# Performance work log

Hardware: AMD Instinct MI355X
Metric: run time of the kernel (lower is better)

The kernel has to match this reference:

```python
import jax, jax.numpy as jnp
import numpy as np

D = 64        # embedding_dim
H = 16        # embedding_dim // 4
DAY = 86400.0
N_USERS = 200000
T_TOTAL = 8400000


def _mlp(x, w1, b1, w2, b2):
    return jax.nn.relu(x @ w1 + b1) @ w2 + b2


def setup_inputs() -> dict:
    key = jax.random.key(0)
    ks = jax.random.split(key, 20)
    N, T = N_USERS, T_TOTAL
    # every user gets >= 3 check-ins, rest assigned randomly
    base = np.tile(np.arange(N, dtype=np.int32), 3)
    rnd = np.asarray(jax.random.randint(ks[0], (T - 3 * N,), 0, N, dtype=jnp.int32))
    segment_ids = jnp.asarray(np.sort(np.concatenate([base, rnd])).astype(np.int32))
    # quantized coordinates so per-user unique-row counting is meaningful
    locations = jnp.round(jax.random.normal(ks[1], (T, 2), jnp.float32) * 50.0) / 50.0
    timestamps = jax.random.uniform(ks[2], (T,), jnp.float32, 0.0, 1.0e7)
    categories = jax.random.randint(ks[3], (T,), 0, 10, dtype=jnp.int32)

    def lin(k, din, dout):
        kw, kb = jax.random.split(k)
        w = jax.random.normal(kw, (din, dout), jnp.float32) / np.float32(np.sqrt(din))
        b = jax.random.normal(kb, (dout,), jnp.float32) * 0.01
        return w, b

    p = {}
    ki = 4
    for nm, din in [("loc", 2), ("tmp", 3), ("act", 10), ("mob", 4)]:
        p[f"w_{nm}1"], p[f"b_{nm}1"] = lin(ks[ki], din, H); ki += 1
        p[f"w_{nm}2"], p[f"b_{nm}2"] = lin(ks[ki], H, H); ki += 1
    p["w_cmb1"], p["b_cmb1"] = lin(ks[ki], D, D); ki += 1
    p["w_cmb2"], p["b_cmb2"] = lin(ks[ki], D, D)
    return dict(locations=locations, timestamps=timestamps,
                categories=categories, segment_ids=segment_ids, num_users=N, **p)


def reference(locations, timestamps,
              w_loc1, b_loc1, w_loc2, b_loc2,
              w_tmp1, b_tmp1, w_tmp2, b_tmp2,
              w_act1, b_act1, w_act2, b_act2,
              w_mob1, b_mob1, w_mob2, b_mob2,
              w_cmb1, b_cmb1, w_cmb2, b_cmb2,
              categories, segment_ids, num_users):
    seg, N = segment_ids, num_users
    ss = lambda v: jax.ops.segment_sum(v, seg, num_segments=N, indices_are_sorted=True)
    L = ss(jnp.ones_like(timestamps))                        # [N] check-ins per user

    # home location = mean over user's locations
    home = ss(locations) / L[:, None]                        # [N, 2]

    # temporal patterns: mean hour / day / month
    hours = jnp.mod(timestamps, DAY) / 3600.0
    days = jnp.mod(timestamps / DAY, 7.0)
    months = jnp.mod(timestamps / (30.0 * DAY), 12.0)
    tmp = ss(jnp.stack([hours, days, months], -1)) / L[:, None]   # [N, 3]

    # activity distribution over 10 POI categories
    hist = jnp.zeros((N, 10), locations.dtype).at[seg, categories].add(1.0)
    hs = hist.sum(-1, keepdims=True)
    act = jnp.where(hs > 0, hist / jnp.maximum(hs, 1.0), hist)    # [N, 10]

    # mobility stats: radius = std (ddof=1) of distance to centroid
    d = jnp.linalg.norm(locations - home[seg], axis=1)
    dmean = ss(d) / L
    radius = jnp.sqrt(ss((d - dmean[seg]) ** 2) / (L - 1.0))

    # diversity: unique locations per user via segment-local lexsort
    x, y = locations[:, 0], locations[:, 1]
    order = jnp.lexsort((y, x, seg))
    sx, sy, sseg = x[order], y[order], seg[order]
    new = jnp.concatenate([jnp.ones((1,), bool),
                           (sseg[1:] != sseg[:-1]) | (sx[1:] != sx[:-1]) | (sy[1:] != sy[:-1])])
    uniq = jax.ops.segment_sum(new.astype(locations.dtype), sseg,
                               num_segments=N, indices_are_sorted=True)
    diversity = uniq / L

    # frequency: check-ins per day of time span
    tmax = jax.ops.segment_max(timestamps, seg, num_segments=N, indices_are_sorted=True)
    tmin = jax.ops.segment_min(timestamps, seg, num_segments=N, indices_are_sorted=True)
    span = (tmax - tmin) / DAY
    freq = L / jnp.maximum(span, 1.0)

    # regularity: 1 / (std(consecutive time diffs, ddof=1) + 1e-6)
    diffs = timestamps[1:] - timestamps[:-1]
    same = seg[1:] == seg[:-1]
    seg1 = seg[1:]
    ss1 = lambda v: jax.ops.segment_sum(v, seg1, num_segments=N, indices_are_sorted=True)
    m = L - 1.0                                              # diffs per user
    dmu = ss1(jnp.where(same, diffs, 0.0)) / m
    dvar = ss1(jnp.where(same, (diffs - dmu[seg1]) ** 2, 0.0)) / (m - 1.0)
    reg = 1.0 / (jnp.sqrt(dvar) + 1e-6)

    mob = jnp.stack([radius, diversity, freq, reg], -1)      # [N, 4]

    feats = jnp.concatenate([
        _mlp(home, w_loc1, b_loc1, w_loc2, b_loc2),
        _mlp(tmp, w_tmp1, b_tmp1, w_tmp2, b_tmp2),
        _mlp(act, w_act1, b_act1, w_act2, b_act2),
        _mlp(mob, w_mob1, b_mob1, w_mob2, b_mob2),
    ], -1)                                                   # [N, 64]
    return _mlp(feats, w_cmb1, b_cmb1, w_cmb2, b_cmb2)       # [N, 64]
```

## Files before the change

kernel.cpp:

```cpp
#include <hip/hip_runtime.h>

typedef short bf16x8 __attribute__((ext_vector_type(8)));
typedef float f32x4 __attribute__((ext_vector_type(4)));

struct Params {
  const float* loc; const float* ts; const int* cat; const int* seg;
  const int* off;
  const float *wl1,*bl1,*wl2,*bl2;
  const float *wt1,*bt1,*wt2,*bt2;
  const float *wa1,*ba1,*wa2,*ba2;
  const float *wm1,*bm1,*wm2,*bm2;
  const float *wc1,*bc1,*wc2,*bc2;
  float* out;
  unsigned* wfrag;
  int N, T, use_off;
};

__global__ void offsets_kernel(const int* __restrict__ seg, int* __restrict__ off, int T, int N) {
  int i = blockIdx.x * blockDim.x + threadIdx.x;
  if (i == 0) off[N] = T;
  if (i < T) {
    int s = seg[i];
    if (i == 0 || seg[i-1] != s) off[s] = i;
  }
}

__device__ __forceinline__ int rdlane_i(int v, int l) {
  return __builtin_amdgcn_readlane(v, l);
}
__device__ __forceinline__ float rdlane_f(float v, int l) {
  return __int_as_float(__builtin_amdgcn_readlane(__float_as_int(v), l));
}

__device__ __forceinline__ unsigned bf16r(float f) {
  unsigned x = __float_as_uint(f);
  return (x + 0x7fffu + ((x >> 16) & 1u)) >> 16;
}
__device__ __forceinline__ unsigned pack_hl(float f) {
  unsigned hi = bf16r(f);
  float r = f - __uint_as_float(hi << 16);
  return (hi << 16) | bf16r(r);
}

__device__ __forceinline__ float exact_fmod(float a, float m, float rcp_m) {
  float q = floorf(a * rcp_m);
  float r = fmaf(q, -m, a);
  if (r < 0.0f) r += m;
  else if (r >= m) r -= m;
  return r;
}

__device__ __forceinline__ f32x4 mfma16(bf16x8 a, bf16x8 b, f32x4 c) {
  return __builtin_amdgcn_mfma_f32_16x16x32_bf16(a, b, c, 0, 0, 0);
}

__device__ __forceinline__ void lda(const unsigned* rp, bf16x8& hi, bf16x8& lo) {
  uint4 w0 = *(const uint4*)rp;
  uint4 w1 = *(const uint4*)(rp + 4);
  union { unsigned u[4]; bf16x8 v; } H, L;
  H.u[0] = __builtin_amdgcn_perm(w0.y, w0.x, 0x07060302u);
  H.u[1] = __builtin_amdgcn_perm(w0.w, w0.z, 0x07060302u);
  H.u[2] = __builtin_amdgcn_perm(w1.y, w1.x, 0x07060302u);
  H.u[3] = __builtin_amdgcn_perm(w1.w, w1.z, 0x07060302u);
  L.u[0] = __builtin_amdgcn_perm(w0.y, w0.x, 0x05040100u);
  L.u[1] = __builtin_amdgcn_perm(w0.w, w0.z, 0x05040100u);
  L.u[2] = __builtin_amdgcn_perm(w1.y, w1.x, 0x05040100u);
  L.u[3] = __builtin_amdgcn_perm(w1.w, w1.z, 0x05040100u);
  hi = H.v; lo = L.v;
}

__device__ __forceinline__ float bdval_(const float* wl2, const float* wt2,
                                        const float* wa2, const float* wm2,
                                        int k, int col) {
  if ((k >> 4) != (col >> 4)) return 0.f;
  int b = col >> 4;
  const float* W2 = (b & 2) ? ((b & 1) ? wm2 : wa2) : ((b & 1) ? wt2 : wl2);
  return W2[(k & 15) * 16 + (col & 15)];
}

__device__ __forceinline__ unsigned frag_word(const Params& p, int m) {
  int fi = m >> 8;
  int ln = (m >> 2) & 63;
  int j2 = m & 3;
  int layer, nt, ks;
  if (fi < 4)       { layer = 0; nt = fi;             ks = nt >> 1; }
  else if (fi < 12) { layer = 1; nt = (fi - 4) >> 1;  ks = (fi - 4) & 1; }
  else              { layer = 2; nt = (fi - 12) >> 1; ks = (fi - 12) & 1; }
  int col = nt * 16 + (ln & 15);
  int k0  = ks * 32 + ((ln >> 4) << 3) + (j2 << 1);
  float v0, v1;
  if (layer == 0) {
    v0 = bdval_(p.wl2, p.wt2, p.wa2, p.wm2, k0, col);
    v1 = bdval_(p.wl2, p.wt2, p.wa2, p.wm2, k0 + 1, col);
  } else {
    const float* W = (layer == 1) ? p.wc1 : p.wc2;
    v0 = W[k0 * 64 + col]; v1 = W[(k0 + 1) * 64 + col];
  }
  return (bf16r(v1) << 16) | bf16r(v0);
}

__global__ void pack_kernel(Params p) {
  int m = blockIdx.x * 256 + threadIdx.x;
  if (m < 5120) p.wfrag[m] = frag_word(p, m);
}

__device__ __forceinline__ bf16x8 g_ldb(const Params& p, int fi, int lane) {
  union { uint4 q; unsigned u[4]; bf16x8 v; } U;
  if (p.wfrag) {
    U.q = *(const uint4*)(p.wfrag + ((fi * 64 + lane) << 2));
  } else {
    int m = fi * 256 + lane * 4;
    U.u[0] = frag_word(p, m + 0);
    U.u[1] = frag_word(p, m + 1);
    U.u[2] = frag_word(p, m + 2);
    U.u[3] = frag_word(p, m + 3);
  }
  return U.v;
}

__device__ __forceinline__ int lower_bound(const int* seg, int T, int v) {
  int lo = 0, hi = T;
  while (lo < hi) { int m = (lo + hi) >> 1; if (seg[m] < v) lo = m + 1; else hi = m; }
  return lo;
}

__device__ __forceinline__ float pscan_f(float v) {
  v += __int_as_float(__builtin_amdgcn_update_dpp(0, __float_as_int(v), 0x111, 0xf, 0xf, true));
  v += __int_as_float(__builtin_amdgcn_update_dpp(0, __float_as_int(v), 0x112, 0xf, 0xf, true));
  v += __int_as_float(__builtin_amdgcn_update_dpp(0, __float_as_int(v), 0x114, 0xf, 0xf, true));
  v += __int_as_float(__builtin_amdgcn_update_dpp(0, __float_as_int(v), 0x118, 0xf, 0xf, true));
  v += __int_as_float(__builtin_amdgcn_update_dpp(0, __float_as_int(v), 0x142, 0xa, 0xf, true));
  v += __int_as_float(__builtin_amdgcn_update_dpp(0, __float_as_int(v), 0x143, 0xc, 0xf, true));
  return v;
}
__device__ __forceinline__ unsigned pscan_u(unsigned v) {
  int x = (int)v;
  x += __builtin_amdgcn_update_dpp(0, x, 0x111, 0xf, 0xf, true);
  x += __builtin_amdgcn_update_dpp(0, x, 0x112, 0xf, 0xf, true);
  x += __builtin_amdgcn_update_dpp(0, x, 0x114, 0xf, 0xf, true);
  x += __builtin_amdgcn_update_dpp(0, x, 0x118, 0xf, 0xf, true);
  x += __builtin_amdgcn_update_dpp(0, x, 0x142, 0xa, 0xf, true);
  x += __builtin_amdgcn_update_dpp(0, x, 0x143, 0xc, 0xf, true);
  return (unsigned)x;
}
__device__ __forceinline__ unsigned wshr1_u(unsigned v) {
  return (unsigned)__builtin_amdgcn_update_dpp(0, (int)v, 0x138, 0xf, 0xf, true);
}
__device__ __forceinline__ float wshr1_f(float v) {
  return __int_as_float(__builtin_amdgcn_update_dpp(0, __float_as_int(v), 0x138, 0xf, 0xf, true));
}

__global__ __launch_bounds__(256, 4) void mobility_kernel(Params p) {
  __shared__ __align__(16) unsigned s_pool[4352];
  __shared__ float s_w1[304];
  __shared__ float s_b1[64], s_b2[64], s_bc1[64], s_bc2[64];

  int tid = threadIdx.x;
  int lane = tid & 63, w = tid >> 6;

  if (tid < 32)  s_w1[tid]       = p.wl1[tid];
  if (tid < 48)  s_w1[32 + tid]  = p.wt1[tid];
  if (tid < 160) s_w1[80 + tid]  = p.wa1[tid];
  if (tid < 64)  s_w1[240 + tid] = p.wm1[tid];
  if (tid < 16) {
    s_b1[tid]    = p.bl1[tid]; s_b1[16+tid] = p.bt1[tid];
    s_b1[32+tid] = p.ba1[tid]; s_b1[48+tid] = p.bm1[tid];
    s_b2[tid]    = p.bl2[tid]; s_b2[16+tid] = p.bt2[tid];
    s_b2[32+tid] = p.ba2[tid]; s_b2[48+tid] = p.bm2[tid];
  }
  if (tid < 64) { s_bc1[tid] = p.bc1[tid]; s_bc2[tid] = p.bc2[tid]; }
  __syncthreads();

  int uw0 = blockIdx.x * 64 + w * 16;
  if (uw0 >= p.N) return;
  int myu = uw0 + lane;
  int myuc = min(myu, p.N - 1);
  int s0, e0;
  if (p.use_off) {
    s0 = p.off[myuc]; e0 = p.off[myuc + 1];
  } else {
    s0 = lower_bound(p.seg, p.T, myuc);
    e0 = lower_bound(p.seg, p.T, myuc + 1);
  }
  int W0 = rdlane_i(s0, 0);
  int W1 = rdlane_i(e0, 15);
  float Lf = (float)(e0 - s0);

  const float2* lp2 = (const float2*)p.loc;
  const float NINF = __int_as_float(0xff800000u);
  const float PINF = __int_as_float(0x7f800000u);

  int aKx = 0, aKy = 0, aXX = 0;
  float aH = 0.f, aDY = 0.f, aT = 0.f, aDF2 = 0.f;
  unsigned aH0 = 0u, aH1 = 0u, aH2 = 0u;

  for (int base = W0; base < W1; base += 64) {
    int e = base + lane;
    bool on = e < W1;
    int ec = on ? e : (W1 - 1);
    int sv = p.seg[ec];
    int sn = (ec + 1 < p.T) ? p.seg[ec + 1] : -2;
    float t  = p.ts[ec];
    float tnx = (ec + 1 < p.T) ? p.ts[ec + 1] : 0.f;
    int c = p.cat[ec];
    float2 xy = lp2[ec];

    unsigned vXY = 0u, vXX = 0u, vH0 = 0u, vH1 = 0u, vH2 = 0u;
    float vH = 0.f, vDY = 0.f, vT = 0.f, vDF2 = 0.f;
    if (on) {
      int kx = (int)lrintf(xy.x * 50.0f);
      int ky = (int)lrintf(xy.y * 50.0f);
      vXY = ((unsigned)(kx + 512) << 16) | (unsigned)(ky + 512);
      vXX = (unsigned)(kx * kx + ky * ky);
      float hr = exact_fmod(t, 86400.0f, 1.0f / 86400.0f);
      vH = hr * (1.0f / 3600.0f);
      float ud = (float)((double)t * (1.0 / 86400.0));
      vDY = exact_fmod(ud, 7.0f, 1.0f / 7.0f);
      vT = t;
      unsigned bit = 1u << ((c & 3) * 8);
      int wsel = c >> 2;
      vH0 = (wsel == 0) ? bit : 0u;
      vH1 = (wsel == 1) ? bit : 0u;
      vH2 = (wsel == 2) ? bit : 0u;
      if (sn == sv) { float dt = tnx - t; vDF2 = dt * dt; }
    }

    unsigned pXY = pscan_u(vXY), pXX = pscan_u(vXX);
    unsigned pH0 = pscan_u(vH0), pH1 = pscan_u(vH1), pH2 = pscan_u(vH2);
    float pH = pscan_f(vH), pDY = pscan_f(vDY), pT = pscan_f(vT), pDF2 = pscan_f(vDF2);

    int lo = min(max(s0 - base, 0), 64);
    int hi = min(max(e0 - base, 0), 64);
    int idx = max(hi - 1, 0);
    unsigned PXY = (unsigned)__shfl((int)pXY, idx);
    unsigned PXX = (unsigned)__shfl((int)pXX, idx);
    unsigned PH0 = (unsigned)__shfl((int)pH0, idx);
    unsigned PH1 = (unsigned)__shfl((int)pH1, idx);
    unsigned PH2 = (unsigned)__shfl((int)pH2, idx);
    float PH = __shfl(pH, idx), PDY = __shfl(pDY, idx);
    float PT = __shfl(pT, idx), PDF2 = __shfl(pDF2, idx);
    unsigned LXY = wshr1_u(PXY), LXX = wshr1_u(PXX);
    unsigned LH0 = wshr1_u(PH0), LH1 = wshr1_u(PH1), LH2 = wshr1_u(PH2);
    float LH = wshr1_f(PH), LDY = wshr1_f(PDY);
    float LT = wshr1_f(PT), LDF2 = wshr1_f(PDF2);

    if (hi > lo) {
      int cnt = hi - lo;
      bool ul_ = lo > 0;
      unsigned dXY = PXY - (ul_ ? LXY : 0u);
      aKx += (int)(dXY >> 16) - (cnt << 9);
      aKy += (int)(dXY & 0xffffu) - (cnt << 9);
      aXX += (int)(PXX - (ul_ ? LXX : 0u));
      aH0 += PH0 - (ul_ ? LH0 : 0u);
      aH1 += PH1 - (ul_ ? LH1 : 0u);
      aH2 += PH2 - (ul_ ? LH2 : 0u);
      aH   += PH   - (ul_ ? LH   : 0.f);
      aDY  += PDY  - (ul_ ? LDY  : 0.f);
      aT   += PT   - (ul_ ? LT   : 0.f);
      aDF2 += PDF2 - (ul_ ? LDF2 : 0.f);
    }
  }

  float hx, hy;
  {
    float sx = (float)aKx / 50.0f, sy = (float)aKy / 50.0f;
    hx = sx / Lf; hy = sy / Lf;
  }

  unsigned* fw = s_pool + w * 1088;
  unsigned* hashp = fw;
  float uqf = 0.f, tmxA = NINF, tmnA = PINF, aD = 0.f;
  for (int uu = 0; uu < 16; ++uu) {
    if (uw0 + uu >= p.N) break;
    int suu = rdlane_i(s0, uu), euu = rdlane_i(e0, uu);
    float hxu = rdlane_f(hx, uu), hyu = rdlane_f(hy, uu);
    int Lu = euu - suu;
    int uq = 0;
    float cmx = NINF, cmn = PINF, dsum = 0.f;
    if (Lu <= 96) {
      hashp[lane] = 0u; hashp[64 + lane] = 0u;
      asm volatile("s_waitcnt lgkmcnt(0)" ::: "memory");
      for (int b2 = suu; b2 < euu; b2 += 64) {
        int i = b2 + lane;
        bool fresh = false;
        if (i < euu) {
          float tv = p.ts[i];
          cmx = fmaxf(cmx, tv); cmn = fminf(cmn, tv);
          float2 xy = lp2[i];
          float dx = xy.x - hxu, dyv = xy.y - hyu;
          dsum += sqrtf(fmaf(dx, dx, dyv * dyv));
          int kx = (int)lrintf(xy.x * 50.0f) + 2048;
          int ky = (int)lrintf(xy.y * 50.0f) + 2048;
          unsigned key = (((unsigned)kx << 12) | (unsigned)ky) + 1u;
          unsigned h = (key * 2654435761u) >> 25;
          while (true) {
            unsigned old = atomicCAS(&hashp[h], 0u, key);
            if (old == 0u) { fresh = true; break; }
            if (old == key) break;
            h = (h + 1) & 127u;
          }
        }
        uq += (int)__popcll(__ballot(fresh));
      }
    } else {
      for (int b2 = suu; b2 < euu; b2 += 64) {
        int i = b2 + lane;
        bool fresh = false;
        if (i < euu) {
          float tv = p.ts[i];
          cmx = fmaxf(cmx, tv); cmn = fminf(cmn, tv);
          float x = p.loc[2*(size_t)i], y = p.loc[2*(size_t)i+1];
          float dx = x - hxu, dyv = y - hyu;
          dsum += sqrtf(fmaf(dx, dx, dyv * dyv));
          fresh = true;
          for (int jj = suu; jj < i; ++jj) {
            if (p.loc[2*(size_t)jj] == x && p.loc[2*(size_t)jj+1] == y) { fresh = false; break; }
          }
        }
        uq += (int)__popcll(__ballot(fresh));
      }
    }
    #pragma unroll
    for (int o = 32; o > 0; o >>= 1) {
      cmx = fmaxf(cmx, __shfl_xor(cmx, o));
      cmn = fminf(cmn, __shfl_xor(cmn, o));
      dsum += __shfl_xor(dsum, o);
    }
    if (lane == uu) { uqf = (float)uq; tmxA = cmx; tmnA = cmn; aD = dsum; }
  }
  asm volatile("s_waitcnt lgkmcnt(0)" ::: "memory");

  int lr = lane & 15, g2 = lane >> 4;
  int us0 = __shfl(s0, lr), ue0 = __shfl(e0, lr);
  float LfU = (float)(ue0 - us0);
  int KX = __shfl(aKx, lr), KY = __shfl(aKy, lr), XX = __shfl(aXX, lr);
  float H_ = __shfl(aH, lr), DY_ = __shfl(aDY, lr);
  float T_ = __shfl(aT, lr), DF2_ = __shfl(aDF2, lr);
  unsigned H0_ = (unsigned)__shfl((int)aH0, lr);
  unsigned H1_ = (unsigned)__shfl((int)aH1, lr);
  unsigned H2_ = (unsigned)__shfl((int)aH2, lr);
  float TMX_ = __shfl(tmxA, lr), TMN_ = __shfl(tmnA, lr);
  float D_ = __shfl(aD, lr), UQ_ = __shfl(uqf, lr);

  unsigned hp16[16];
  if (g2 == 0) {
    float sxU = (float)KX / 50.0f, syU = (float)KY / 50.0f;
    float hxU = sxU / LfU, hyU = syU / LfU;
    #pragma unroll
    for (int j = 0; j < 16; ++j)
      hp16[j] = pack_hl(fmaxf(s_b1[j] + hxU * s_w1[j] + hyU * s_w1[16 + j], 0.f));
  } else if (g2 == 1) {
    float th = H_ / LfU, tdy = DY_ / LfU;
    float tmo = (T_ * (1.0f / 2592000.0f)) / LfU;
    #pragma unroll
    for (int j = 0; j < 16; ++j)
      hp16[j] = pack_hl(fmaxf(s_b1[16 + j] + th * s_w1[32 + j] + tdy * s_w1[48 + j]
                              + tmo * s_w1[64 + j], 0.f));
  } else if (g2 == 2) {
    float act[10];
    act[0] = (float)(H0_ & 255u) / LfU;
    act[1] = (float)((H0_ >> 8) & 255u) / LfU;
    act[2] = (float)((H0_ >> 16) & 255u) / LfU;
    act[3] = (float)((H0_ >> 24) & 255u) / LfU;
    act[4] = (float)(H1_ & 255u) / LfU;
    act[5] = (float)((H1_ >> 8) & 255u) / LfU;
    act[6] = (float)((H1_ >> 16) & 255u) / LfU;
    act[7] = (float)((H1_ >> 24) & 255u) / LfU;
    act[8] = (float)(H2_ & 255u) / LfU;
    act[9] = (float)((H2_ >> 8) & 255u) / LfU;
    #pragma unroll
    for (int j = 0; j < 16; ++j) {
      float aa = s_b1[32 + j];
      #pragma unroll
      for (int b = 0; b < 10; ++b) aa = fmaf(act[b], s_w1[80 + b * 16 + j], aa);
      hp16[j] = pack_hl(fmaxf(aa, 0.f));
    }
  } else {
    float sxU = (float)KX / 50.0f, syU = (float)KY / 50.0f;
    float sxx = (float)XX / 2500.0f;
    float sD = D_;
    float sD2 = sxx - (sxU * sxU + syU * syU) / LfU;
    float varD = (sD2 - sD * sD / LfU) / (LfU - 1.0f);
    float rad  = sqrtf(fmaxf(varD, 0.0f));
    float divy = UQ_ / LfU;
    float span = (TMX_ - TMN_) / 86400.0f;
    float freq = LfU / fmaxf(span, 1.0f);
    float tfirst = p.ts[us0];
    float tlast  = p.ts[ue0 - 1];
    float sdf = tlast - tfirst;
    float mm   = LfU - 1.0f;
    float dmu  = sdf / mm;
    float dvar = (DF2_ - mm * dmu * dmu) / (mm - 1.0f);
    float reg  = 1.0f / (sqrtf(fmaxf(dvar, 0.0f)) + 1e-6f);
    #pragma unroll
    for (int j = 0; j < 16; ++j)
      hp16[j] = pack_hl(fmaxf(s_b1[48 + j] + rad * s_w1[240 + j] + divy * s_w1[256 + j]
                              + freq * s_w1[272 + j] + reg * s_w1[288 + j], 0.f));
  }

  {
    unsigned* row = fw + lr * 68 + g2 * 16;
    #pragma unroll
    for (int j = 0; j < 4; ++j)
      *(uint4*)(row + 4 * j) = make_uint4(hp16[4*j], hp16[4*j+1], hp16[4*j+2], hp16[4*j+3]);
  }
  asm volatile("s_waitcnt lgkmcnt(0)" ::: "memory");

  int lg = lane >> 4;
  const unsigned* arow = fw + lr * 68 + (lg << 3);

  bf16x8 ah[2], al[2];
  lda(arow,      ah[0], al[0]);
  lda(arow + 32, ah[1], al[1]);
  f32x4 acc[4];
  #pragma unroll
  for (int nt = 0; nt < 4; ++nt) {
    float bv = s_b2[nt * 16 + lr];
    acc[nt] = (f32x4){bv, bv, bv, bv};
    int ks = nt >> 1;
    bf16x8 bw = g_ldb(p, nt, lane);
    acc[nt] = mfma16(ah[ks], bw, acc[nt]);
    acc[nt] = mfma16(al[ks], bw, acc[nt]);
  }
  #pragma unroll
  for (int nt = 0; nt < 4; ++nt)
    #pragma unroll
    for (int r = 0; r < 4; ++r)
      fw[(lg * 4 + r) * 68 + nt * 16 + lr] = pack_hl(acc[nt][r]);
  asm volatile("s_waitcnt lgkmcnt(0)" ::: "memory");

  lda(arow,      ah[0], al[0]);
  lda(arow + 32, ah[1], al[1]);
  #pragma unroll
  for (int nt = 0; nt < 4; ++nt) {
    float bv = s_bc1[nt * 16 + lr];
    acc[nt] = (f32x4){bv, bv, bv, bv};
    #pragma unroll
    for (int ks = 0; ks < 2; ++ks) {
      bf16x8 bw = g_ldb(p, 4 + nt * 2 + ks, lane);
      acc[nt] = mfma16(ah[ks], bw, acc[nt]);
      acc[nt] = mfma16(al[ks], bw, acc[nt]);
    }
  }
  #pragma unroll
  for (int nt = 0; nt < 4; ++nt)
    #pragma unroll
    for (int r = 0; r < 4; ++r)
      fw[(lg * 4 + r) * 68 + nt * 16 + lr] = pack_hl(fmaxf(acc[nt][r], 0.f));
  asm volatile("s_waitcnt lgkmcnt(0)" ::: "memory");

  lda(arow,      ah[0], al[0]);
  lda(arow + 32, ah[1], al[1]);
  #pragma unroll
  for (int nt = 0; nt < 4; ++nt) {
    float bv = s_bc2[nt * 16 + lr];
    acc[nt] = (f32x4){bv, bv, bv, bv};
    #pragma unroll
    for (int ks = 0; ks < 2; ++ks) {
      bf16x8 bw = g_ldb(p, 12 + nt * 2 + ks, lane);
      acc[nt] = mfma16(ah[ks], bw, acc[nt]);
      acc[nt] = mfma16(al[ks], bw, acc[nt]);
    }
  }
  #pragma unroll
  for (int nt = 0; nt < 4; ++nt)
    #pragma unroll
    for (int r = 0; r < 4; ++r) {
      int uo = uw0 + lg * 4 + r;
      if (uo < p.N) p.out[(size_t)uo * 64 + nt * 16 + lr] = acc[nt][r];
    }
}

extern "C" void kernel_launch(void* const* d_in, const int* in_sizes, int n_in,
                              void* d_out, int out_size, void* d_ws, size_t ws_size,
                              hipStream_t stream) {
  Params p;
  p.loc = (const float*)d_in[0];
  p.ts  = (const float*)d_in[1];
  p.cat = (const int*)d_in[2];
  p.seg = (const int*)d_in[3];
  p.wl1 = (const float*)d_in[5];  p.bl1 = (const float*)d_in[6];
  p.wl2 = (const float*)d_in[7];  p.bl2 = (const float*)d_in[8];
  p.wt1 = (const float*)d_in[9];  p.bt1 = (const float*)d_in[10];
  p.wt2 = (const float*)d_in[11]; p.bt2 = (const float*)d_in[12];
  p.wa1 = (const float*)d_in[13]; p.ba1 = (const float*)d_in[14];
  p.wa2 = (const float*)d_in[15]; p.ba2 = (const float*)d_in[16];
  p.wm1 = (const float*)d_in[17]; p.bm1 = (const float*)d_in[18];
  p.wm2 = (const float*)d_in[19]; p.bm2 = (const float*)d_in[20];
  p.wc1 = (const float*)d_in[21]; p.bc1 = (const float*)d_in[22];
  p.wc2 = (const float*)d_in[23]; p.bc2 = (const float*)d_in[24];
  p.out = (float*)d_out;
  p.N = out_size / 64;
  p.T = in_sizes[1];
  int* off = (int*)d_ws;
  p.off = off;
  p.use_off = (ws_size >= (size_t)(p.N + 1) * sizeof(int)) ? 1 : 0;

  size_t fragOff = (((size_t)p.N + 1) + 3) & ~(size_t)3;
  p.wfrag = nullptr;
  if (ws_size >= (fragOff + 5120) * sizeof(unsigned)) {
    p.wfrag = (unsigned*)d_ws + fragOff;
    pack_kernel<<<20, 256, 0, stream>>>(p);
  }

  if (p.use_off) {
    offsets_kernel<<<(p.T + 255)/256, 256, 0, stream>>>(p.seg, off, p.T, p.N);
  }
  int nblocks = (p.N + 63) / 64;
  mobility_kernel<<<nblocks, 256, 0, stream>>>(p);
}
```

Measured before the change: 177.0 us.

## Process two users per wavefront in half-waves and reuse loaded neighbors via DPP

```diff
diff --git a/kernel.cpp b/kernel.cpp
--- a/kernel.cpp
+++ b/kernel.cpp
@@ -149,6 +149,9 @@
 __device__ __forceinline__ float wshr1_f(float v) {
   return __int_as_float(__builtin_amdgcn_update_dpp(0, __float_as_int(v), 0x138, 0xf, 0xf, true));
 }
+__device__ __forceinline__ int wshr1_i(int v) {
+  return __builtin_amdgcn_update_dpp(0, v, 0x138, 0xf, 0xf, true);
+}
 
 __global__ __launch_bounds__(256, 4) void mobility_kernel(Params p) {
   __shared__ __align__(16) unsigned s_pool[4352];
@@ -194,16 +197,21 @@
   float aH = 0.f, aDY = 0.f, aT = 0.f, aDF2 = 0.f;
   unsigned aH0 = 0u, aH1 = 0u, aH2 = 0u;
 
+  int carry_sv = -987654;
+  float carry_t = 0.f;
+
   for (int base = W0; base < W1; base += 64) {
     int e = base + lane;
     bool on = e < W1;
     int ec = on ? e : (W1 - 1);
     int sv = p.seg[ec];
-    int sn = (ec + 1 < p.T) ? p.seg[ec + 1] : -2;
     float t  = p.ts[ec];
-    float tnx = (ec + 1 < p.T) ? p.ts[ec + 1] : 0.f;
     int c = p.cat[ec];
     float2 xy = lp2[ec];
+
+    int psv = wshr1_i(sv);
+    float pt = wshr1_f(t);
+    if (lane == 0) { psv = carry_sv; pt = carry_t; }
 
     unsigned vXY = 0u, vXX = 0u, vH0 = 0u, vH1 = 0u, vH2 = 0u;
     float vH = 0.f, vDY = 0.f, vT = 0.f, vDF2 = 0.f;
@@ -222,7 +230,7 @@
       vH0 = (wsel == 0) ? bit : 0u;
       vH1 = (wsel == 1) ? bit : 0u;
       vH2 = (wsel == 2) ? bit : 0u;
-      if (sn == sv) { float dt = tnx - t; vDF2 = dt * dt; }
+      if (psv == sv) { float dt = t - pt; vDF2 = dt * dt; }
     }
 
     unsigned pXY = pscan_u(vXY), pXX = pscan_u(vXX);
@@ -259,6 +267,9 @@
       aT   += PT   - (ul_ ? LT   : 0.f);
       aDF2 += PDF2 - (ul_ ? LDF2 : 0.f);
     }
+
+    carry_sv = rdlane_i(sv, 63);
+    carry_t  = rdlane_f(t, 63);
   }
 
   float hx, hy;
@@ -268,65 +279,79 @@
   }
 
   unsigned* fw = s_pool + w * 1088;
-  unsigned* hashp = fw;
   float uqf = 0.f, tmxA = NINF, tmnA = PINF, aD = 0.f;
-  for (int uu = 0; uu < 16; ++uu) {
-    if (uw0 + uu >= p.N) break;
-    int suu = rdlane_i(s0, uu), euu = rdlane_i(e0, uu);
-    float hxu = rdlane_f(hx, uu), hyu = rdlane_f(hy, uu);
-    int Lu = euu - suu;
-    int uq = 0;
-    float cmx = NINF, cmn = PINF, dsum = 0.f;
-    if (Lu <= 96) {
-      hashp[lane] = 0u; hashp[64 + lane] = 0u;
-      asm volatile("s_waitcnt lgkmcnt(0)" ::: "memory");
-      for (int b2 = suu; b2 < euu; b2 += 64) {
-        int i = b2 + lane;
-        bool fresh = false;
-        if (i < euu) {
-          float tv = p.ts[i];
-          cmx = fmaxf(cmx, tv); cmn = fminf(cmn, tv);
-          float2 xy = lp2[i];
-          float dx = xy.x - hxu, dyv = xy.y - hyu;
-          dsum += sqrtf(fmaf(dx, dx, dyv * dyv));
-          int kx = (int)lrintf(xy.x * 50.0f) + 2048;
-          int ky = (int)lrintf(xy.y * 50.0f) + 2048;
-          unsigned key = (((unsigned)kx << 12) | (unsigned)ky) + 1u;
-          unsigned h = (key * 2654435761u) >> 25;
-          while (true) {
-            unsigned old = atomicCAS(&hashp[h], 0u, key);
-            if (old == 0u) { fresh = true; break; }
-            if (old == key) break;
-            h = (h + 1) & 127u;
+  {
+    int g  = lane >> 5;
+    int li = lane & 31;
+    unsigned* hashp = fw + g * 128;
+    for (int uu = 0; uu < 8; ++uu) {
+      int gu = 2 * uu + g;
+      bool uvalid = (uw0 + gu) < p.N;
+      int suu = __shfl(s0, gu), euu = __shfl(e0, gu);
+      float hxu = __shfl(hx, gu), hyu = __shfl(hy, gu);
+      int Lu = euu - suu;
+      int uq = 0;
+      float cmx = NINF, cmn = PINF, dsum = 0.f;
+      if (uvalid) {
+        if (Lu <= 96) {
+          hashp[li] = 0u; hashp[32 + li] = 0u; hashp[64 + li] = 0u; hashp[96 + li] = 0u;
+          asm volatile("s_waitcnt lgkmcnt(0)" ::: "memory");
+          for (int b2 = suu; b2 < euu; b2 += 32) {
+            int i = b2 + li;
+            bool fresh = false;
+            if (i < euu) {
+              float tv = p.ts[i];
+              cmx = fmaxf(cmx, tv); cmn = fminf(cmn, tv);
+              float2 xy = lp2[i];
+              float dx = xy.x - hxu, dyv = xy.y - hyu;
+              dsum += sqrtf(fmaf(dx, dx, dyv * dyv));
+              int kx = (int)lrintf(xy.x * 50.0f) + 2048;
+              int ky = (int)lrintf(xy.y * 50.0f) + 2048;
+              unsigned key = (((unsigned)kx << 12) | (unsigned)ky) + 1u;
+              unsigned h = (key * 2654435761u) >> 25;
+              while (true) {
+                unsigned old = atomicCAS(&hashp[h], 0u, key);
+                if (old == 0u) { fresh = true; break; }
+                if (old == key) break;
+                h = (h + 1) & 127u;
+              }
+            }
+            unsigned long long bm = __ballot(fresh);
+            uq += __popc((unsigned)(bm >> (g * 32)));
+          }
+        } else {
+          for (int b2 = suu; b2 < euu; b2 += 32) {
+            int i = b2 + li;
+            bool fresh = false;
+            if (i < euu) {
+              float tv = p.ts[i];
+              cmx = fmaxf(cmx, tv); cmn = fminf(cmn, tv);
+              float x = p.loc[2*(size_t)i], y = p.loc[2*(size_t)i+1];
+              float dx = x - hxu, dyv = y - hyu;
+              dsum += sqrtf(fmaf(dx, dx, dyv * dyv));
+              fresh = true;
+              for (int jj = suu; jj < i; ++jj) {
+                if (p.loc[2*(size_t)jj] == x && p.loc[2*(size_t)jj+1] == y) { fresh = false; break; }
+              }
+            }
+            unsigned long long bm = __ballot(fresh);
+            uq += __popc((unsigned)(bm >> (g * 32)));
           }
         }
-        uq += (int)__popcll(__ballot(fresh));
       }
-    } else {
-      for (int b2 = suu; b2 < euu; b2 += 64) {
-        int i = b2 + lane;
-        bool fresh = false;
-        if (i < euu) {
-          float tv = p.ts[i];
-          cmx = fmaxf(cmx, tv); cmn = fminf(cmn, tv);
-          float x = p.loc[2*(size_t)i], y = p.loc[2*(size_t)i+1];
-          float dx = x - hxu, dyv = y - hyu;
-          dsum += sqrtf(fmaf(dx, dx, dyv * dyv));
-          fresh = true;
-          for (int jj = suu; jj < i; ++jj) {
-            if (p.loc[2*(size_t)jj] == x && p.loc[2*(size_t)jj+1] == y) { fresh = false; break; }
-          }
-        }
-        uq += (int)__popcll(__ballot(fresh));
+      #pragma unroll
+      for (int o = 16; o > 0; o >>= 1) {
+        cmx = fmaxf(cmx, __shfl_xor(cmx, o));
+        cmn = fminf(cmn, __shfl_xor(cmn, o));
+        dsum += __shfl_xor(dsum, o);
       }
-    }
-    #pragma unroll
-    for (int o = 32; o > 0; o >>= 1) {
-      cmx = fmaxf(cmx, __shfl_xor(cmx, o));
-      cmn = fminf(cmn, __shfl_xor(cmn, o));
-      dsum += __shfl_xor(dsum, o);
-    }
-    if (lane == uu) { uqf = (float)uq; tmxA = cmx; tmnA = cmn; aD = dsum; }
+      int srcl = (lane & 1) << 5;
+      float mxv = __shfl(cmx, srcl);
+      float mnv = __shfl(cmn, srcl);
+      float dsv = __shfl(dsum, srcl);
+      int   uqv = __shfl(uq, srcl);
+      if ((lane >> 1) == uu) { tmxA = mxv; tmnA = mnv; aD = dsv; uqf = (float)uqv; }
+    }
   }
   asm volatile("s_waitcnt lgkmcnt(0)" ::: "memory");
 
```

New measurement: 163.9 us. 1.08x faster.
